# Optimization experiments

Measured on AMD Instinct MI355X. Metric: run time of the kernel, lower is better.

## Reference

```python
import jax, jax.numpy as jnp
import numpy as np

N, CIN, T, V, COUT = 64, 64, 256, 25, 128
CI = COUT // 2  # inter_channels
EPS = 1e-5


def setup_inputs() -> dict:
    key = jax.random.key(0)
    ks = jax.random.split(key, 12)
    s = 0.05
    d = {}
    d['x'] = jax.random.normal(ks[0], (N, CIN, T, V), jnp.float32)
    d['A'] = jax.random.normal(ks[1], (3, V, V), jnp.float32) * s
    d['Al'] = jax.random.normal(ks[2], (3, V, V), jnp.float32) * s
    d['Wp'] = jax.random.normal(ks[3], (3, COUT, CIN), jnp.float32) * s
    d['bp'] = jnp.zeros((3, COUT), jnp.float32)
    d['Wm1'] = jax.random.normal(ks[4], (CI, CIN), jnp.float32) * s
    d['bm1'] = jnp.zeros((CI,), jnp.float32)
    d['Wm2'] = jax.random.normal(ks[5], (CI, CIN), jnp.float32) * s
    d['bm2'] = jnp.zeros((CI,), jnp.float32)
    d['Wm3'] = jax.random.normal(ks[6], (COUT, CI), jnp.float32) * s
    d['bm3'] = jnp.zeros((COUT,), jnp.float32)
    d['Wm4'] = jax.random.normal(ks[7], (COUT, CIN), jnp.float32) * s
    d['bm4'] = jnp.zeros((COUT,), jnp.float32)
    d['alpha'] = jax.random.normal(ks[8], (1,), jnp.float32) * s
    d['bn_gamma'] = jnp.ones((COUT,), jnp.float32)
    d['bn_beta'] = jnp.zeros((COUT,), jnp.float32)
    d['down_W'] = jax.random.normal(ks[9], (COUT, CIN), jnp.float32) * s
    d['down_gamma'] = jnp.ones((COUT,), jnp.float32)
    d['down_beta'] = jnp.zeros((COUT,), jnp.float32)
    return d


def _bn_train(y, gamma, beta):
    # BatchNorm2d training forward: biased batch stats over (N, T, V)
    mu = jnp.mean(y, axis=(0, 2, 3), keepdims=True)
    var = jnp.var(y, axis=(0, 2, 3), keepdims=True)
    return (y - mu) * jax.lax.rsqrt(var + EPS) * gamma[None, :, None, None] + beta[None, :, None, None]


def reference(x, A, Al, Wp, bp, Wm1, bm1, Wm2, bm2, Wm3, bm3, Wm4, bm4,
              alpha, bn_gamma, bn_beta, down_W, down_gamma, down_beta):
    Tn = x.shape[2]
    # --- static graph branch: sum over 3 subsets of (A+Al) graph matmuls ---
    Xp = jnp.einsum('soi,nitv->snotv', Wp, x) + bp[:, None, :, None, None]  # (3,N,COUT,T,V)
    y = jnp.einsum('suv,snctv->nctu', A + Al, Xp)                           # (N,COUT,T,V)
    # --- dynamic adjacency from temporal-difference features ---
    xf = jnp.mean(jnp.einsum('oi,nitv->notv', Wm1, x[:, :, :Tn - 2]) + bm1[None, :, None, None], axis=2)  # (N,CI,V)
    xb = jnp.mean(jnp.einsum('oi,nitv->notv', Wm2, x[:, :, 2:]) + bm2[None, :, None, None], axis=2)       # (N,CI,V)
    diff = xb[:, :, :, None] - xf[:, :, None, :]                            # (N,CI,V,V)
    Rd = jnp.tanh(jnp.einsum('oi,nivw->novw', Wm3, diff) + bm3[None, :, None, None])  # (N,COUT,V,V)
    Xm = jnp.einsum('oi,nitv->notv', Wm4, x) + bm4[None, :, None, None]     # (N,COUT,T,V)
    z = jnp.einsum('ncuv,nctv->nctu', Rd, Xm)                               # (N,COUT,T,V)
    y = z * alpha + y
    # --- BN, residual (1x1 conv + BN down-path since CIN != COUT), ReLU ---
    y = _bn_train(y, bn_gamma, bn_beta)
    d = jnp.einsum('oi,nitv->notv', down_W, x)  # no bias
    d = _bn_train(d, down_gamma, down_beta)
    return jax.nn.relu(y + d)
```

## Files before the change

### kernel.cpp

```cpp
#include <hip/hip_runtime.h>
#include <stdint.h>

typedef unsigned short u16;
typedef unsigned int   u32;
typedef short bf16x8 __attribute__((ext_vector_type(8)));
typedef float f32x4  __attribute__((ext_vector_type(4)));

#define N_    64
#define CIN_  64
#define T_    256
#define V_    25
#define COUT_ 128
#define CI_   64
#define EPS_  1e-5f
#define CNT_  409600.0f

#define MFMA16(a,b,c) __builtin_amdgcn_mfma_f32_16x16x32_bf16((a),(b),(c),0,0,0)

__device__ __forceinline__ u16 f2bf(float f) {
  u32 u = __float_as_uint(f);
  u += 0x7fffu + ((u >> 16) & 1u);
  return (u16)(u >> 16);
}
__device__ __forceinline__ float bf2f(u16 h) { return __uint_as_float(((u32)h) << 16); }

__global__ __launch_bounds__(256) void k_pack(const float* __restrict__ Wp, const float* __restrict__ Wm4,
                                              const float* __restrict__ dW, const float* __restrict__ A,
                                              const float* __restrict__ Al,
                                              u16* __restrict__ w5, u16* __restrict__ bst,
                                              float* __restrict__ rsumw) {
  int tid = threadIdx.x;
  for (int i = tid; i < 640 * 64; i += 256) {
    int r = i >> 6, k = i & 63;
    float v = (r < 384) ? Wp[i] : (r < 512) ? Wm4[(r - 384) * 64 + k] : dW[(r - 512) * 64 + k];
    w5[i] = f2bf(v);
  }
  for (int i = tid; i < 3 * 32 * 32; i += 256) {
    int s = i >> 10, rem = i & 1023, u = rem >> 5, v = rem & 31;
    float val = (u < 25 && v < 25) ? (A[(s * 25 + u) * 25 + v] + Al[(s * 25 + u) * 25 + v]) : 0.f;
    bst[i] = f2bf(val);
  }
  if (tid < 75) {
    int s = tid / 25, u = tid % 25;
    float acc = 0.f;
    for (int v = 0; v < 25; v++) acc += A[(s * 25 + u) * 25 + v] + Al[(s * 25 + u) * 25 + v];
    rsumw[tid] = acc;
  }
}

__global__ __launch_bounds__(256) void k_means(const float* __restrict__ x,
                                               float* __restrict__ mf, float* __restrict__ mb) {
  int i = blockIdx.x, n = blockIdx.y;
  const float* src = x + ((size_t)n * CIN_ + i) * T_ * V_;
  __shared__ float xs[T_ * V_];
  __shared__ float pf[8][32], pb[8][32];
  {
    float4* xs4 = (float4*)xs;
    const float4* src4 = (const float4*)src;
    for (int idx = threadIdx.x; idx < (T_ * V_) / 4; idx += 256) xs4[idx] = src4[idx];
  }
  __syncthreads();
  int v = threadIdx.x & 31, g = threadIdx.x >> 5;
  float sf = 0.f, sb = 0.f;
  if (v < V_) {
    for (int t = g; t < T_; t += 8) {
      float val = xs[t * V_ + v];
      if (t < T_ - 2) sf += val;
      if (t >= 2)     sb += val;
    }
  }
  pf[g][v] = sf; pb[g][v] = sb;
  __syncthreads();
  if (threadIdx.x < V_) {
    float af = 0.f, ab = 0.f;
    for (int gg = 0; gg < 8; gg++) { af += pf[gg][threadIdx.x]; ab += pb[gg][threadIdx.x]; }
    size_t o = ((size_t)n * CIN_ + i) * V_ + threadIdx.x;
    mf[o] = af * (1.0f / 254.0f);
    mb[o] = ab * (1.0f / 254.0f);
  }
}

__global__ __launch_bounds__(256) void k_rd1(
    const float* __restrict__ mf, const float* __restrict__ mb,
    const float* __restrict__ Wm1, const float* __restrict__ bm1,
    const float* __restrict__ Wm2, const float* __restrict__ bm2,
    const float* __restrict__ Wm3, float* __restrict__ pqws) {
  int n = blockIdx.x, tid = threadIdx.x;
  __shared__ float MfL[CIN_][V_], MbL[CIN_][V_], xfL[CI_][V_], xbL[CI_][V_];
  for (int idx = tid; idx < CIN_ * V_; idx += 256) {
    MfL[idx / V_][idx % V_] = mf[(size_t)n * CIN_ * V_ + idx];
    MbL[idx / V_][idx % V_] = mb[(size_t)n * CIN_ * V_ + idx];
  }
  __syncthreads();
  for (int idx = tid; idx < CI_ * V_; idx += 256) {
    int o = idx / V_, v = idx % V_;
    float af = bm1[o], ab = bm2[o];
    for (int i = 0; i < CIN_; i++) {
      af += Wm1[o * CIN_ + i] * MfL[i][v];
      ab += Wm2[o * CIN_ + i] * MbL[i][v];
    }
    xfL[o][v] = af; xbL[o][v] = ab;
  }
  __syncthreads();
  for (int idx = tid; idx < COUT_ * V_; idx += 256) {
    int c = idx / V_, u = idx % V_;
    float p = 0.f, q = 0.f;
    for (int i = 0; i < CI_; i++) {
      p += Wm3[c * CI_ + i] * xbL[i][u];
      q += Wm3[c * CI_ + i] * xfL[i][u];
    }
    pqws[(size_t)n * 6400 + idx] = p;
    pqws[(size_t)n * 6400 + 3200 + idx] = q;
  }
}

__global__ __launch_bounds__(256) void k_rd2(
    const float* __restrict__ pqws, const float* __restrict__ rsumw,
    const float* __restrict__ bm3, const float* __restrict__ bm4,
    const float* __restrict__ bp, const float* __restrict__ alpha,
    u16* __restrict__ rdws, float* __restrict__ biasws) {
  int cg = blockIdx.x, n = blockIdx.y;
  int c0 = cg * 16, tid = threadIdx.x;
  __shared__ float Ps[400], Qs[400], rs[75];
  for (int idx = tid; idx < 400; idx += 256) {
    Ps[idx] = pqws[(size_t)n * 6400 + c0 * 25 + idx];
    Qs[idx] = pqws[(size_t)n * 6400 + 3200 + c0 * 25 + idx];
  }
  if (tid < 75) rs[tid] = rsumw[tid];
  __syncthreads();
  float al = alpha[0];
  for (int r = tid; r < 400; r += 256) {
    int cl = r / 25, u = r - cl * 25, c = c0 + cl;
    float pv = Ps[r] + bm3[c];
    float acc = 0.f;
    u16* dst = rdws + ((size_t)(n * COUT_ + c) * 25 + u) * 32;
    for (int w0 = 0; w0 < 25; w0++) {
      float val = al * tanhf(pv - Qs[cl * 25 + w0]);
      dst[w0] = f2bf(val);
      acc += val;
    }
    for (int w0 = 25; w0 < 32; w0++) dst[w0] = 0;
    float yb = 0.f;
    for (int s = 0; s < 3; s++) yb += bp[s * COUT_ + c] * rs[s * 25 + u];
    biasws[(size_t)(n * COUT_ + c) * 25 + u] = bm4[c] * acc + yb;
  }
}

__global__ __launch_bounds__(512, 4) void k_main(
    const float* __restrict__ x, const u16* __restrict__ w5, const u16* __restrict__ bst,
    const u16* __restrict__ rdws, const float* __restrict__ biasws,
    u16* __restrict__ out16, float* __restrict__ partials) {
  __shared__ __align__(16) char smem[36864];
  __shared__ u16 dls[16 * 408];
  __shared__ float statsL[512];
  const int tid = threadIdx.x;
  const int w = tid >> 6, l = tid & 63;
  const int lc = l & 15, lq = l >> 4;
  const int n = blockIdx.y, tc = blockIdx.x, t0 = tc * 16;

  bf16x8 bw[3][2];
  #pragma unroll
  for (int s = 0; s < 3; s++)
    #pragma unroll
    for (int ut = 0; ut < 2; ut++)
      bw[s][ut] = *(const bf16x8*)(bst + (s * 32 + ut * 16 + lc) * 32 + lq * 8);

  bf16x8 xf[4][2] = {};
  const float* xb = x + (size_t)n * CIN_ * T_ * V_ + (size_t)t0 * V_;
  #pragma unroll
  for (int ks = 0; ks < 2; ks++) {
    u32* xslw = (u32*)smem;
    for (int idx = tid; idx < 16 * 416; idx += 512) {
      int i2 = idx / 416, p = idx - i2 * 416;
      float a = 0.f, b = 0.f;
      int ch = ks * 32 + 2 * i2;
      if (p < 400) {
        a = xb[(size_t)ch       * (T_ * V_) + p];
        b = xb[(size_t)(ch + 1) * (T_ * V_) + p];
      }
      int f = (p ^ (p >> 2)) & 3;
      xslw[p * 16 + (i2 ^ (f << 2))] = ((u32)f2bf(b) << 16) | (u32)f2bf(a);
    }
    __syncthreads();
    #pragma unroll
    for (int pi = 0; pi < 4; pi++) {
      int pt = w + pi * 8;
      if (pt < 26) {
        int p = pt * 16 + lc;
        int f = (p ^ (p >> 2)) & 3;
        xf[pi][ks] = *(const bf16x8*)((const u16*)smem + p * 32 + ((lq ^ f) << 3));
      }
    }
    __syncthreads();
  }

  {
    uint4 z4 = {0, 0, 0, 0};
    uint4* q = (uint4*)smem;
    for (int idx = tid; idx < 2304; idx += 512) q[idx] = z4;
    statsL[tid] = 0.f;
  }
  __syncthreads();

  u16* xpl = (u16*)smem;
  const f32x4 zz = {0.f, 0.f, 0.f, 0.f};
  u32* out32 = (u32*)out16;

  for (int g = 0; g < 8; g++) {
    const int c0 = g * 16;
    f32x4 acc[2][2];
    #pragma unroll
    for (int cl = 0; cl < 2; cl++) { acc[cl][0] = zz; acc[cl][1] = zz; }

    #pragma unroll
    for (int h = 0; h < 2; h++) {
      const int nsl = h ? 3 : 2;
      bf16x8 af[3][2];
      #pragma unroll
      for (int si = 0; si < 3; si++) if (si < nsl) {
        int sl = h * 2 + si;
        #pragma unroll
        for (int ks = 0; ks < 2; ks++)
          af[si][ks] = *(const bf16x8*)(w5 + ((sl * 128 + c0 + lc) * 64 + ks * 32 + lq * 8));
      }
      #pragma unroll
      for (int si = 0; si < 3; si++) if (si < nsl) {
        int sl = h * 2 + si;
        #pragma unroll
        for (int pi = 0; pi < 4; pi++) {
          int pt = w + pi * 8;
          if (pt >= 26) continue;
          f32x4 pa = MFMA16(af[si][0], xf[pi][0], zz);
          pa = MFMA16(af[si][1], xf[pi][1], pa);
          int p = pt * 16 + lc;
          if (p < 400) {
            u32 up = (u32)p, t = up / 25u, v = up - t * 25u;
            if (sl < 4) {
              int slot = sl & 1;
              u16* dst = xpl + (4 * lq) * 1152 + t * 72 + slot * 32 + v;
              #pragma unroll
              for (int r = 0; r < 4; r++) dst[r * 1152] = f2bf(pa[r]);
            } else {
              u16* dd = dls + (4 * lq) * 408 + p;
              #pragma unroll
              for (int r = 0; r < 4; r++) dd[r * 408] = f2bf(pa[r]);
            }
          }
        }
      }
      __syncthreads();

      {
        bf16x8 rdf0[2], rdf1[2];
        if (h == 1) {
          #pragma unroll
          for (int cl = 0; cl < 2; cl++) {
            size_t rb = (size_t)(n * COUT_ + c0 + w * 2 + cl) * 25;
            rdf0[cl] = *(const bf16x8*)(rdws + (rb + lc) * 32 + lq * 8);
            int u1c = (lc + 16 < 25) ? lc + 16 : 24;
            rdf1[cl] = *(const bf16x8*)(rdws + (rb + u1c) * 32 + lq * 8);
          }
        }
        #pragma unroll
        for (int cl = 0; cl < 2; cl++) {
          int clocal = w * 2 + cl;
          #pragma unroll
          for (int kl = 0; kl < 2; kl++) {
            bf16x8 aX = *(const bf16x8*)(xpl + clocal * 1152 + lc * 72 + kl * 32 + lq * 8);
            int kk = h * 2 + kl;
            bf16x8 b0, b1;
            if (kk < 3) { b0 = bw[kk][0]; b1 = bw[kk][1]; }
            else        { b0 = rdf0[cl];  b1 = rdf1[cl]; }
            acc[cl][0] = MFMA16(aX, b0, acc[cl][0]);
            acc[cl][1] = MFMA16(aX, b1, acc[cl][1]);
          }
        }
      }
      if (h == 1) {
        #pragma unroll
        for (int cl = 0; cl < 2; cl++) {
          int c = c0 + w * 2 + cl;
          size_t bb = (size_t)(n * COUT_ + c) * 25;
          float bias0 = biasws[bb + lc];
          int u1 = lc + 16; bool v1 = u1 < 25;
          float bias1 = biasws[bb + (v1 ? u1 : 24)];
          size_t ob = ((size_t)(n * COUT_ + c) * T_ + t0) * V_;
          const u16* dd = dls + (w * 2 + cl) * 408;
          float sy = 0.f, sq = 0.f, sd = 0.f, sdd = 0.f;
          #pragma unroll
          for (int r = 0; r < 4; r++) {
            int t = 4 * lq + r;
            float y0 = acc[cl][0][r] + bias0;
            u16 d0 = dd[t * 25 + lc];
            out32[ob + t * 25 + lc] = ((u32)d0 << 16) | (u32)f2bf(y0);
            sy += y0; sq += y0 * y0;
            float f0 = bf2f(d0); sd += f0; sdd += f0 * f0;
            if (v1) {
              float y1 = acc[cl][1][r] + bias1;
              u16 d1 = dd[t * 25 + u1];
              out32[ob + t * 25 + u1] = ((u32)d1 << 16) | (u32)f2bf(y1);
              sy += y1; sq += y1 * y1;
              float f1 = bf2f(d1); sd += f1; sdd += f1 * f1;
            }
          }
          #pragma unroll
          for (int off = 1; off < 64; off <<= 1) {
            sy += __shfl_xor(sy, off); sq += __shfl_xor(sq, off);
            sd += __shfl_xor(sd, off); sdd += __shfl_xor(sdd, off);
          }
          if (l == 0) {
            atomicAdd(&statsL[c * 4 + 0], sy); atomicAdd(&statsL[c * 4 + 1], sq);
            atomicAdd(&statsL[c * 4 + 2], sd); atomicAdd(&statsL[c * 4 + 3], sdd);
          }
        }
      }
      __syncthreads();
    }
  }
  int bflat = blockIdx.y * 16 + blockIdx.x;
  for (int j = tid; j < 512; j += 512) partials[(size_t)j * 1024 + bflat] = statsL[j];
}

__global__ __launch_bounds__(256) void k_stats1(const float* __restrict__ partials, float* __restrict__ colsum) {
  int w = threadIdx.x >> 6, l = threadIdx.x & 63;
  for (int ci = 0; ci < 8; ci++) {
    int j = blockIdx.x * 32 + w * 8 + ci;
    float s = 0.f;
    for (int it = 0; it < 16; it++) s += partials[(size_t)j * 1024 + it * 64 + l];
    #pragma unroll
    for (int off = 1; off < 64; off <<= 1) s += __shfl_xor(s, off);
    if (l == 0) colsum[j] = s;
  }
}

__global__ __launch_bounds__(128) void k_stats2(
    const float* __restrict__ colsum,
    const float* __restrict__ bn_g, const float* __restrict__ bn_b,
    const float* __restrict__ dn_g, const float* __restrict__ dn_b,
    float* __restrict__ params) {
  int c = threadIdx.x;
  float sy = colsum[c * 4], syy = colsum[c * 4 + 1], sd = colsum[c * 4 + 2], sdd = colsum[c * 4 + 3];
  float muY = sy / CNT_, varY = syy / CNT_ - muY * muY;
  float muD = sd / CNT_, varD = sdd / CNT_ - muD * muD;
  float sY = bn_g[c] * rsqrtf(varY + EPS_);
  float sD = dn_g[c] * rsqrtf(varD + EPS_);
  float off = bn_b[c] - muY * sY + dn_b[c] - muD * sD;
  params[c * 4 + 0] = sY; params[c * 4 + 1] = sD; params[c * 4 + 2] = off;
}

__global__ __launch_bounds__(256) void k_final(u32* __restrict__ io, const float* __restrict__ params) {
  int slab = blockIdx.x;
  int c = slab & (COUT_ - 1);
  float sY = params[c * 4], sD = params[c * 4 + 1], off = params[c * 4 + 2];
  uint4* io4 = (uint4*)io + (size_t)slab * 1600;
  #pragma unroll
  for (int j = 0; j < 7; j++) {
    int idx = j * 256 + (int)threadIdx.x;
    if (idx < 1600) {
      uint4 wv = io4[idx];
      uint4 o;
      o.x = __float_as_uint(fmaxf(fmaf(bf2f((u16)(wv.x & 0xffffu)), sY, fmaf(bf2f((u16)(wv.x >> 16)), sD, off)), 0.f));
      o.y = __float_as_uint(fmaxf(fmaf(bf2f((u16)(wv.y & 0xffffu)), sY, fmaf(bf2f((u16)(wv.y >> 16)), sD, off)), 0.f));
      o.z = __float_as_uint(fmaxf(fmaf(bf2f((u16)(wv.z & 0xffffu)), sY, fmaf(bf2f((u16)(wv.z >> 16)), sD, off)), 0.f));
      o.w = __float_as_uint(fmaxf(fmaf(bf2f((u16)(wv.w & 0xffffu)), sY, fmaf(bf2f((u16)(wv.w >> 16)), sD, off)), 0.f));
      io4[idx] = o;
    }
  }
}

extern "C" void kernel_launch(void* const* d_in, const int* in_sizes, int n_in,
                              void* d_out, int out_size, void* d_ws, size_t ws_size,
                              hipStream_t stream) {
  const float* x    = (const float*)d_in[0];
  const float* A    = (const float*)d_in[1];
  const float* Al   = (const float*)d_in[2];
  const float* Wp   = (const float*)d_in[3];
  const float* bp   = (const float*)d_in[4];
  const float* Wm1  = (const float*)d_in[5];
  const float* bm1  = (const float*)d_in[6];
  const float* Wm2  = (const float*)d_in[7];
  const float* bm2  = (const float*)d_in[8];
  const float* Wm3  = (const float*)d_in[9];
  const float* bm3  = (const float*)d_in[10];
  const float* Wm4  = (const float*)d_in[11];
  const float* bm4  = (const float*)d_in[12];
  const float* alpha= (const float*)d_in[13];
  const float* bn_g = (const float*)d_in[14];
  const float* bn_b = (const float*)d_in[15];
  const float* dW   = (const float*)d_in[16];
  const float* dn_g = (const float*)d_in[17];
  const float* dn_b = (const float*)d_in[18];

  char* ws = (char*)d_ws;
  float* mf       = (float*)(ws + 0);
  float* mb       = (float*)(ws + 409600);
  u16*   rdws     = (u16*)  (ws + 819200);
  float* biasws   = (float*)(ws + 13926400);
  u16*   w5       = (u16*)  (ws + 14745600);
  u16*   bstw     = (u16*)  (ws + 14827520);
  float* partials = (float*)(ws + 14833664);
  float* colsum   = (float*)(ws + 16930816);
  float* params   = (float*)(ws + 16932864);
  float* pqws  = partials;
  float* rsumw = colsum;

  k_pack <<<dim3(1),       dim3(256), 0, stream>>>(Wp, Wm4, dW, A, Al, w5, bstw, rsumw);
  k_means<<<dim3(64, 64),  dim3(256), 0, stream>>>(x, mf, mb);
  k_rd1  <<<dim3(64),      dim3(256), 0, stream>>>(mf, mb, Wm1, bm1, Wm2, bm2, Wm3, pqws);
  k_rd2  <<<dim3(8, 64),   dim3(256), 0, stream>>>(pqws, rsumw, bm3, bm4, bp, alpha, rdws, biasws);
  k_main <<<dim3(16, 64),  dim3(512), 0, stream>>>(x, w5, bstw, rdws, biasws,
                                                   (u16*)d_out, partials);
  k_stats1<<<dim3(16),     dim3(256), 0, stream>>>(partials, colsum);
  k_stats2<<<dim3(1),      dim3(128), 0, stream>>>(colsum, bn_g, bn_b, dn_g, dn_b, params);
  k_final<<<dim3(64 * 128),dim3(256), 0, stream>>>((u32*)d_out, params);
}
```

Measured before the change: 673.3 us.

## Stage all four graph slices in one swizzled LDS buffer, halve k_main barriers

k_main used to project slices in two halves, with a barrier and an MFMA pass after each. It now projects all five weight slices at once into a larger XOR-swizzled LDS layout (64 KB) and runs a single 4-step K accumulation per channel group. This cuts the syncthreads per group from four to two and is meant to reduce LDS bank conflicts. It also hoists index math and rd/bias loads, and spreads k_pack across 8 blocks. The larger LDS footprint may lower occupancy from the requested 4 blocks per CU.

```diff
diff --git a/kernel.cpp b/kernel.cpp
--- a/kernel.cpp
+++ b/kernel.cpp
@@ -29,22 +29,23 @@
                                               const float* __restrict__ Al,
                                               u16* __restrict__ w5, u16* __restrict__ bst,
                                               float* __restrict__ rsumw) {
-  int tid = threadIdx.x;
-  for (int i = tid; i < 640 * 64; i += 256) {
+  int tid = blockIdx.x * 256 + threadIdx.x;
+  int stride = gridDim.x * 256;
+  for (int i = tid; i < 640 * 64; i += stride) {
     int r = i >> 6, k = i & 63;
     float v = (r < 384) ? Wp[i] : (r < 512) ? Wm4[(r - 384) * 64 + k] : dW[(r - 512) * 64 + k];
     w5[i] = f2bf(v);
   }
-  for (int i = tid; i < 3 * 32 * 32; i += 256) {
+  for (int i = tid; i < 3 * 32 * 32; i += stride) {
     int s = i >> 10, rem = i & 1023, u = rem >> 5, v = rem & 31;
     float val = (u < 25 && v < 25) ? (A[(s * 25 + u) * 25 + v] + Al[(s * 25 + u) * 25 + v]) : 0.f;
     bst[i] = f2bf(val);
   }
-  if (tid < 75) {
-    int s = tid / 25, u = tid % 25;
+  if (blockIdx.x == 0 && threadIdx.x < 75) {
+    int s = threadIdx.x / 25, u = threadIdx.x % 25;
     float acc = 0.f;
     for (int v = 0; v < 25; v++) acc += A[(s * 25 + u) * 25 + v] + Al[(s * 25 + u) * 25 + v];
-    rsumw[tid] = acc;
+    rsumw[threadIdx.x] = acc;
   }
 }
 
@@ -150,8 +151,8 @@
     const float* __restrict__ x, const u16* __restrict__ w5, const u16* __restrict__ bst,
     const u16* __restrict__ rdws, const float* __restrict__ biasws,
     u16* __restrict__ out16, float* __restrict__ partials) {
-  __shared__ __align__(16) char smem[36864];
-  __shared__ u16 dls[16 * 408];
+  __shared__ __align__(16) char smem[65536];
+  __shared__ u16 dls[16 * 400];
   __shared__ float statsL[512];
   const int tid = threadIdx.x;
   const int w = tid >> 6, l = tid & 63;
@@ -194,10 +195,26 @@
     __syncthreads();
   }
 
+  bool pvalid[4]; int wbase[4], txm[4], vhi[4], dlsp[4];
+  #pragma unroll
+  for (int pi = 0; pi < 4; pi++) {
+    int pt = w + pi * 8;
+    pvalid[pi] = (pt < 25);
+    int p = pt * 16 + lc;
+    u32 up = (u32)p, t = up / 25u, v = up - t * 25u;
+    wbase[pi] = (int)(t * 128u + (v & 7u));
+    txm[pi]   = (int)(t & 15u);
+    vhi[pi]   = (int)(v >> 3);
+    dlsp[pi]  = p;
+  }
+  const int u1 = lc + 16;
+  const bool v1 = (u1 < 25);
+  const int u1c = v1 ? u1 : 24;
+
   {
     uint4 z4 = {0, 0, 0, 0};
     uint4* q = (uint4*)smem;
-    for (int idx = tid; idx < 2304; idx += 512) q[idx] = z4;
+    for (int idx = tid; idx < 4096; idx += 512) q[idx] = z4;
     statsL[tid] = 0.f;
   }
   __syncthreads();
@@ -213,112 +230,87 @@
     for (int cl = 0; cl < 2; cl++) { acc[cl][0] = zz; acc[cl][1] = zz; }
 
     #pragma unroll
-    for (int h = 0; h < 2; h++) {
-      const int nsl = h ? 3 : 2;
-      bf16x8 af[3][2];
+    for (int si = 0; si < 5; si++) {
+      const u16* wrow = w5 + (size_t)(si * 128 + c0 + lc) * 64;
+      bf16x8 af0 = *(const bf16x8*)(wrow + lq * 8);
+      bf16x8 af1 = *(const bf16x8*)(wrow + 32 + lq * 8);
       #pragma unroll
-      for (int si = 0; si < 3; si++) if (si < nsl) {
-        int sl = h * 2 + si;
-        #pragma unroll
-        for (int ks = 0; ks < 2; ks++)
-          af[si][ks] = *(const bf16x8*)(w5 + ((sl * 128 + c0 + lc) * 64 + ks * 32 + lq * 8));
-      }
+      for (int pi = 0; pi < 4; pi++) {
+        if (!pvalid[pi]) continue;
+        f32x4 pa = MFMA16(af0, xf[pi][0], zz);
+        pa = MFMA16(af1, xf[pi][1], pa);
+        if (si < 4) {
+          int chunk = ((si * 4 + vhi[pi]) ^ txm[pi]) << 3;
+          u16* dst = xpl + (4 * lq) * 2048 + wbase[pi] + chunk;
+          #pragma unroll
+          for (int r = 0; r < 4; r++) dst[r * 2048] = f2bf(pa[r]);
+        } else {
+          u16* dd = dls + (4 * lq) * 400 + dlsp[pi];
+          #pragma unroll
+          for (int r = 0; r < 4; r++) dd[r * 400] = f2bf(pa[r]);
+        }
+      }
+    }
+
+    bf16x8 rdf0[2], rdf1[2];
+    float bias0[2], bias1[2];
+    #pragma unroll
+    for (int cl = 0; cl < 2; cl++) {
+      size_t rb = (size_t)(n * COUT_ + c0 + w * 2 + cl) * 25;
+      rdf0[cl] = *(const bf16x8*)(rdws + (rb + lc) * 32 + lq * 8);
+      rdf1[cl] = *(const bf16x8*)(rdws + (rb + u1c) * 32 + lq * 8);
+      size_t bb = (size_t)(n * COUT_ + c0 + w * 2 + cl) * 25;
+      bias0[cl] = biasws[bb + lc];
+      bias1[cl] = biasws[bb + u1c];
+    }
+    __syncthreads();
+
+    #pragma unroll
+    for (int cl = 0; cl < 2; cl++) {
+      int clocal = w * 2 + cl;
       #pragma unroll
-      for (int si = 0; si < 3; si++) if (si < nsl) {
-        int sl = h * 2 + si;
-        #pragma unroll
-        for (int pi = 0; pi < 4; pi++) {
-          int pt = w + pi * 8;
-          if (pt >= 26) continue;
-          f32x4 pa = MFMA16(af[si][0], xf[pi][0], zz);
-          pa = MFMA16(af[si][1], xf[pi][1], pa);
-          int p = pt * 16 + lc;
-          if (p < 400) {
-            u32 up = (u32)p, t = up / 25u, v = up - t * 25u;
-            if (sl < 4) {
-              int slot = sl & 1;
-              u16* dst = xpl + (4 * lq) * 1152 + t * 72 + slot * 32 + v;
-              #pragma unroll
-              for (int r = 0; r < 4; r++) dst[r * 1152] = f2bf(pa[r]);
-            } else {
-              u16* dd = dls + (4 * lq) * 408 + p;
-              #pragma unroll
-              for (int r = 0; r < 4; r++) dd[r * 408] = f2bf(pa[r]);
-            }
-          }
+      for (int kk = 0; kk < 4; kk++) {
+        bf16x8 aX = *(const bf16x8*)(xpl + clocal * 2048 + lc * 128 + (((kk * 4 + lq) ^ lc) << 3));
+        bf16x8 b0, b1;
+        if (kk < 3) { b0 = bw[kk][0]; b1 = bw[kk][1]; }
+        else        { b0 = rdf0[cl];  b1 = rdf1[cl]; }
+        acc[cl][0] = MFMA16(aX, b0, acc[cl][0]);
+        acc[cl][1] = MFMA16(aX, b1, acc[cl][1]);
+      }
+      int c = c0 + clocal;
+      size_t ob = ((size_t)(n * COUT_ + c) * T_ + t0) * V_;
+      const u16* dd = dls + clocal * 400;
+      float sy = 0.f, sq = 0.f, sd = 0.f, sdd = 0.f;
+      #pragma unroll
+      for (int r = 0; r < 4; r++) {
+        int t = 4 * lq + r;
+        float y0 = acc[cl][0][r] + bias0[cl];
+        u16 d0 = dd[t * 25 + lc];
+        out32[ob + t * 25 + lc] = ((u32)d0 << 16) | (u32)f2bf(y0);
+        sy += y0; sq += y0 * y0;
+        float f0 = bf2f(d0); sd += f0; sdd += f0 * f0;
+        if (v1) {
+          float y1 = acc[cl][1][r] + bias1[cl];
+          u16 d1 = dd[t * 25 + u1];
+          out32[ob + t * 25 + u1] = ((u32)d1 << 16) | (u32)f2bf(y1);
+          sy += y1; sq += y1 * y1;
+          float f1 = bf2f(d1); sd += f1; sdd += f1 * f1;
         }
       }
-      __syncthreads();
-
-      {
-        bf16x8 rdf0[2], rdf1[2];
-        if (h == 1) {
-          #pragma unroll
-          for (int cl = 0; cl < 2; cl++) {
-            size_t rb = (size_t)(n * COUT_ + c0 + w * 2 + cl) * 25;
-            rdf0[cl] = *(const bf16x8*)(rdws + (rb + lc) * 32 + lq * 8);
-            int u1c = (lc + 16 < 25) ? lc + 16 : 24;
-            rdf1[cl] = *(const bf16x8*)(rdws + (rb + u1c) * 32 + lq * 8);
-          }
-        }
-        #pragma unroll
-        for (int cl = 0; cl < 2; cl++) {
-          int clocal = w * 2 + cl;
-          #pragma unroll
-          for (int kl = 0; kl < 2; kl++) {
-            bf16x8 aX = *(const bf16x8*)(xpl + clocal * 1152 + lc * 72 + kl * 32 + lq * 8);
-            int kk = h * 2 + kl;
-            bf16x8 b0, b1;
-            if (kk < 3) { b0 = bw[kk][0]; b1 = bw[kk][1]; }
-            else        { b0 = rdf0[cl];  b1 = rdf1[cl]; }
-            acc[cl][0] = MFMA16(aX, b0, acc[cl][0]);
-            acc[cl][1] = MFMA16(aX, b1, acc[cl][1]);
-          }
-        }
-      }
-      if (h == 1) {
-        #pragma unroll
-        for (int cl = 0; cl < 2; cl++) {
-          int c = c0 + w * 2 + cl;
-          size_t bb = (size_t)(n * COUT_ + c) * 25;
-          float bias0 = biasws[bb + lc];
-          int u1 = lc + 16; bool v1 = u1 < 25;
-          float bias1 = biasws[bb + (v1 ? u1 : 24)];
-          size_t ob = ((size_t)(n * COUT_ + c) * T_ + t0) * V_;
-          const u16* dd = dls + (w * 2 + cl) * 408;
-          float sy = 0.f, sq = 0.f, sd = 0.f, sdd = 0.f;
-          #pragma unroll
-          for (int r = 0; r < 4; r++) {
-            int t = 4 * lq + r;
-            float y0 = acc[cl][0][r] + bias0;
-            u16 d0 = dd[t * 25 + lc];
-            out32[ob + t * 25 + lc] = ((u32)d0 << 16) | (u32)f2bf(y0);
-            sy += y0; sq += y0 * y0;
-            float f0 = bf2f(d0); sd += f0; sdd += f0 * f0;
-            if (v1) {
-              float y1 = acc[cl][1][r] + bias1;
-              u16 d1 = dd[t * 25 + u1];
-              out32[ob + t * 25 + u1] = ((u32)d1 << 16) | (u32)f2bf(y1);
-              sy += y1; sq += y1 * y1;
-              float f1 = bf2f(d1); sd += f1; sdd += f1 * f1;
-            }
-          }
-          #pragma unroll
-          for (int off = 1; off < 64; off <<= 1) {
-            sy += __shfl_xor(sy, off); sq += __shfl_xor(sq, off);
-            sd += __shfl_xor(sd, off); sdd += __shfl_xor(sdd, off);
-          }
-          if (l == 0) {
-            atomicAdd(&statsL[c * 4 + 0], sy); atomicAdd(&statsL[c * 4 + 1], sq);
-            atomicAdd(&statsL[c * 4 + 2], sd); atomicAdd(&statsL[c * 4 + 3], sdd);
-          }
-        }
-      }
-      __syncthreads();
-    }
+      #pragma unroll
+      for (int off = 1; off < 64; off <<= 1) {
+        sy += __shfl_xor(sy, off); sq += __shfl_xor(sq, off);
+        sd += __shfl_xor(sd, off); sdd += __shfl_xor(sdd, off);
+      }
+      if (l == 0) {
+        atomicAdd(&statsL[c * 4 + 0], sy); atomicAdd(&statsL[c * 4 + 1], sq);
+        atomicAdd(&statsL[c * 4 + 2], sd); atomicAdd(&statsL[c * 4 + 3], sdd);
+      }
+    }
+    __syncthreads();
   }
   int bflat = blockIdx.y * 16 + blockIdx.x;
-  for (int j = tid; j < 512; j += 512) partials[(size_t)j * 1024 + bflat] = statsL[j];
+  partials[(size_t)tid * 1024 + bflat] = statsL[tid];
 }
 
 __global__ __launch_bounds__(256) void k_stats1(const float* __restrict__ partials, float* __restrict__ colsum) {
@@ -404,7 +396,7 @@
   float* pqws  = partials;
   float* rsumw = colsum;
 
-  k_pack <<<dim3(1),       dim3(256), 0, stream>>>(Wp, Wm4, dW, A, Al, w5, bstw, rsumw);
+  k_pack <<<dim3(8),       dim3(256), 0, stream>>>(Wp, Wm4, dW, A, Al, w5, bstw, rsumw);
   k_means<<<dim3(64, 64),  dim3(256), 0, stream>>>(x, mf, mb);
   k_rd1  <<<dim3(64),      dim3(256), 0, stream>>>(mf, mb, Wm1, bm1, Wm2, bm2, Wm3, pqws);
   k_rd2  <<<dim3(8, 64),   dim3(256), 0, stream>>>(pqws, rsumw, bm3, bm4, bp, alpha, rdws, biasws);
```

Result: faster. 632.1 us (-6.1%).
